# Kernel tuning notes

Measured on AMD Instinct MI355X. Metric: run time of the kernel, lower is better.

The kernel has to match this reference:

```python
import jax, jax.numpy as jnp
import numpy as np

B, S, H, D_IN, DEPTH, NPHN = 128, 1024, 256, 84, 2, 40
N_HEADS = 9  # phn, word1-3, utt1-5
EPS = 1e-5


def setup_inputs() -> dict:
    key = jax.random.key(0)
    ks = jax.random.split(key, 12)
    sc = 0.02
    x = jax.random.normal(ks[0], (B, S, D_IN), jnp.float32)
    # contiguous valid prefix then -1 padding (matches get_last_valid's assumption)
    lengths = jax.random.randint(ks[1], (B,), 1, S + 1)
    phn_vals = jax.random.randint(ks[2], (B, S), 0, NPHN - 1)
    phn = jnp.where(jnp.arange(S)[None, :] < lengths[:, None], phn_vals, -1)
    return {
        "x": x,
        "phn": phn,
        "in_proj_w": jax.random.normal(ks[3], (H, D_IN), jnp.float32) * sc,
        "in_proj_b": jnp.zeros((H,), jnp.float32),
        "phn_proj_w": jax.random.normal(ks[4], (H, NPHN), jnp.float32) * sc,
        "phn_proj_b": jnp.zeros((H,), jnp.float32),
        "w_ih": jax.random.normal(ks[5], (DEPTH, 4 * H, H), jnp.float32) * sc,
        "w_hh": jax.random.normal(ks[6], (DEPTH, 4 * H, H), jnp.float32) * sc,
        "b_ih": jnp.zeros((DEPTH, 4 * H), jnp.float32),
        "b_hh": jnp.zeros((DEPTH, 4 * H), jnp.float32),
        "ln_g": jnp.ones((N_HEADS, H), jnp.float32),
        "ln_b": jnp.zeros((N_HEADS, H), jnp.float32),
        "head_w": jax.random.normal(ks[7], (N_HEADS, H), jnp.float32) * sc,
        "head_b": jnp.zeros((N_HEADS,), jnp.float32),
    }


def _lstm(h0, w_ih, w_hh, b_ih, b_hh):
    # h0: [B,S,H]; torch gate order i,f,g,o
    seq = jnp.transpose(h0, (1, 0, 2))  # [S,B,H]
    b = h0.shape[0]
    for layer in range(DEPTH):
        Wih, Whh = w_ih[layer], w_hh[layer]
        bias = b_ih[layer] + b_hh[layer]

        def step(carry, xt, Wih=Wih, Whh=Whh, bias=bias):
            hp, cp = carry
            g = xt @ Wih.T + hp @ Whh.T + bias
            i, f, gg, o = jnp.split(g, 4, axis=-1)
            c = jax.nn.sigmoid(f) * cp + jax.nn.sigmoid(i) * jnp.tanh(gg)
            hn = jax.nn.sigmoid(o) * jnp.tanh(c)
            return (hn, c), hn

        init = (jnp.zeros((b, H), h0.dtype), jnp.zeros((b, H), h0.dtype))
        _, seq = jax.lax.scan(step, init, seq)
    return jnp.transpose(seq, (1, 0, 2))  # [B,S,H]


def reference(x, phn, in_proj_w, in_proj_b, phn_proj_w, phn_proj_b,
              w_ih, w_hh, b_ih, b_hh, ln_g, ln_b, head_w, head_b):
    b, s = x.shape[0], x.shape[1]
    mask = phn >= 0  # [B,S]
    phn_oh = jax.nn.one_hot(phn + 1, NPHN, dtype=x.dtype)
    h = (x @ in_proj_w.T + in_proj_b) + (phn_oh @ phn_proj_w.T + phn_proj_b)
    hidden = _lstm(h, w_ih, w_hh, b_ih, b_hh)  # [B,S,H]

    # All 9 heads share the LN-normalized activations; fold gamma/beta into the
    # per-head linear: score_k = <xhat, gamma_k*w_k> + <beta_k, w_k> + b_k
    mu = hidden.mean(-1, keepdims=True)
    var = ((hidden - mu) ** 2).mean(-1, keepdims=True)
    xhat = (hidden - mu) * jax.lax.rsqrt(var + EPS)
    scores = (jnp.einsum('bsh,kh->bsk', xhat, ln_g * head_w)
              + (ln_b * head_w).sum(-1) + head_b)  # [B,S,9]

    # last valid token per sequence: index before first mask==0 (or S-1 if all valid)
    first_inv = jnp.argmax(~mask, axis=1)
    idx = jnp.where(mask.all(axis=1), s - 1, first_inv - 1)  # [B]
    last = scores[jnp.arange(b), idx]  # [B,9]

    p = scores[..., 0:1]
    w1, w2, w3 = scores[..., 1:2], scores[..., 2:3], scores[..., 3:4]
    u1, u2, u3, u4, u5 = (last[:, 4 + k][:, None] for k in range(5))
    return (u1, u2, u3, u4, u5, p, w1, w2, w3)
```

## Files before the change

kernel.cpp:

```cpp
#include <hip/hip_runtime.h>


typedef _Float16 h2    __attribute__((ext_vector_type(2)));
typedef _Float16 f16x8 __attribute__((ext_vector_type(8)));
typedef float    f32x4 __attribute__((ext_vector_type(4)));

#define NW_MAT 262144

static __device__ __forceinline__ float fdot2u(unsigned int w, unsigned int h, float c){
#if defined(__has_builtin) && __has_builtin(__builtin_amdgcn_fdot2)
  return __builtin_amdgcn_fdot2(__builtin_bit_cast(h2, w), __builtin_bit_cast(h2, h), c, false);
#else
  h2 a = __builtin_bit_cast(h2, w), b = __builtin_bit_cast(h2, h);
  return c + (float)a[0]*(float)b[0] + (float)a[1]*(float)b[1];
#endif
}
static __device__ __forceinline__ float sigmf(float x){ return 1.f/(1.f + __expf(-x)); }
static __device__ __forceinline__ float tanhf_(float x){ return 1.f - 2.f/(__expf(2.f*x) + 1.f); }

__global__ void k_prep(const float* __restrict__ w_ih, const float* __restrict__ w_hh,
                       const float* __restrict__ b_ih, const float* __restrict__ b_hh,
                       const float* __restrict__ ln_g, const float* __restrict__ ln_b,
                       const float* __restrict__ head_w, const float* __restrict__ head_b,
                       _Float16* wih0, _Float16* whh0, _Float16* wih1, _Float16* whh1,
                       float* bias0, float* bias1, float* vk, float* ck)
{
  int i = blockIdx.x*256 + threadIdx.x;
  if (i < NW_MAT){
    wih0[i] = (_Float16)w_ih[i];
    whh0[i] = (_Float16)w_hh[i];
    wih1[i] = (_Float16)w_ih[NW_MAT + i];
    whh1[i] = (_Float16)w_hh[NW_MAT + i];
  }
  if (i < 1024){
    bias0[i] = b_ih[i]        + b_hh[i];
    bias1[i] = b_ih[1024 + i] + b_hh[1024 + i];
  }
  if (i < 2304) vk[i] = ln_g[i]*head_w[i];
  if (i < 9){
    float s = 0.f;
    for (int h = 0; h < 256; ++h) s += ln_b[i*256 + h]*head_w[i*256 + h];
    ck[i] = s + head_b[i];
  }
}

__global__ void k_idx(const int* __restrict__ phn, int* __restrict__ idx)
{
  int b = blockIdx.x, l = threadIdx.x;
  int found = -1;
  for (int t0 = 0; t0 < 1024; t0 += 64){
    int v = phn[b*1024 + t0 + l];
    unsigned long long m = __ballot(v < 0);
    if (m){ found = t0 + (__ffsll(m) - 1); break; }
  }
  if (l == 0) idx[b] = (found < 0) ? 1023 : found - 1;
}

__global__ void k_embed(const float* __restrict__ x, const int* __restrict__ phn,
                        const float* __restrict__ ipw, const float* __restrict__ ipb,
                        const float* __restrict__ ppw, const float* __restrict__ ppb,
                        _Float16* __restrict__ E, int Tc, int LT, int tc0)
{
  __shared__ float xs[8][84];
  __shared__ int pv[8];
  int tid = threadIdx.x;
  int m0 = blockIdx.x * 8;
  for (int i = tid; i < 8*84; i += 256){
    int r = i/84, k = i - r*84;
    int m = m0 + r; int b = m >> LT; int t = tc0 + (m & (Tc-1));
    xs[r][k] = x[((size_t)b*1024 + t)*84 + k];
  }
  if (tid < 8){
    int m = m0 + tid; int b = m >> LT; int t = tc0 + (m & (Tc-1));
    pv[tid] = phn[b*1024 + t];
  }
  __syncthreads();
  float acc[8] = {0.f,0.f,0.f,0.f,0.f,0.f,0.f,0.f};
  const float* wrow = ipw + tid*84;
  for (int k = 0; k < 84; ++k){
    float wv = wrow[k];
    #pragma unroll
    for (int r = 0; r < 8; ++r) acc[r] += wv * xs[r][k];
  }
  float base = ipb[tid] + ppb[tid];
  #pragma unroll
  for (int r = 0; r < 8; ++r){
    float e = acc[r] + base + ppw[tid*40 + (pv[r] + 1)];
    E[(size_t)(m0 + r)*256 + tid] = (_Float16)e;
  }
}

__global__ __launch_bounds__(256) void k_gemm(const _Float16* __restrict__ A,
                                              const _Float16* __restrict__ Bw,
                                              const float* __restrict__ bias,
                                              _Float16* __restrict__ C)
{
  __shared__ __align__(16) _Float16 lA[128*64];
  __shared__ __align__(16) _Float16 lB[128*64];
  int tid = threadIdx.x;
  int tm = blockIdx.x, tn = blockIdx.y;
  int l = tid & 63, w = tid >> 6;
  int wm = w >> 1, wn = w & 1;
  f32x4 acc[4][4];
  #pragma unroll
  for (int mi = 0; mi < 4; ++mi)
    #pragma unroll
    for (int ni = 0; ni < 4; ++ni) acc[mi][ni] = (f32x4){0.f,0.f,0.f,0.f};
  int rr = tid >> 3, cc = tid & 7;
  #pragma unroll 1
  for (int kb = 0; kb < 4; ++kb){
    uint4 av[4], bv[4];
    #pragma unroll
    for (int i = 0; i < 4; ++i){
      int r = rr + 32*i;
      av[i] = *(const uint4*)(A  + ((size_t)(tm*128 + r))*256 + kb*64 + cc*8);
      bv[i] = *(const uint4*)(Bw + ((size_t)(tn*128 + r))*256 + kb*64 + cc*8);
    }
    __syncthreads();
    #pragma unroll
    for (int i = 0; i < 4; ++i){
      int r = rr + 32*i;
      *(uint4*)&lA[r*64 + cc*8] = av[i];
      *(uint4*)&lB[r*64 + cc*8] = bv[i];
    }
    __syncthreads();
    #pragma unroll
    for (int kk = 0; kk < 2; ++kk){
      f16x8 aF[4], bF[4];
      #pragma unroll
      for (int mi = 0; mi < 4; ++mi)
        aF[mi] = *(const f16x8*)&lA[(wm*64 + mi*16 + (l&15))*64 + kk*32 + (l>>4)*8];
      #pragma unroll
      for (int ni = 0; ni < 4; ++ni)
        bF[ni] = *(const f16x8*)&lB[(wn*64 + ni*16 + (l&15))*64 + kk*32 + (l>>4)*8];
      #pragma unroll
      for (int mi = 0; mi < 4; ++mi)
        #pragma unroll
        for (int ni = 0; ni < 4; ++ni)
          acc[mi][ni] = __builtin_amdgcn_mfma_f32_16x16x32_f16(aF[mi], bF[ni], acc[mi][ni], 0, 0, 0);
    }
  }
  #pragma unroll
  for (int mi = 0; mi < 4; ++mi){
    #pragma unroll
    for (int ni = 0; ni < 4; ++ni){
      int n = tn*128 + wn*64 + ni*16 + (l & 15);
      float bn = bias[n];
      #pragma unroll
      for (int j = 0; j < 4; ++j){
        int m = tm*128 + wm*64 + mi*16 + (l>>4)*4 + j;
        C[(size_t)m*1024 + n] = (_Float16)(acc[mi][ni][j] + bn);
      }
    }
  }
}

__global__ __launch_bounds__(512, 2) void k_lstm(const _Float16* __restrict__ G,
                                                 const _Float16* __restrict__ W,
                                                 _Float16* __restrict__ Hout,
                                                 float* __restrict__ h_state,
                                                 float* __restrict__ c_state,
                                                 int Tc, int first)
{
  __shared__ __align__(16) unsigned int h_pk_s[128];
  __shared__ float gf[1024];
  __shared__ __align__(16) unsigned int wlds[32768];
  int tid = threadIdx.x;
  int b = blockIdx.x;
  int r0 = 2*tid, r1 = r0 + 1;
  const uint4* w0s = (const uint4*)(W + (size_t)r0*256);
  const uint4* w1s = (const uint4*)(W + (size_t)r1*256);
  uint4 w0v[24], w1v[24];
  #pragma unroll
  for (int c2 = 0; c2 < 24; ++c2){ w0v[c2] = w0s[c2]; w1v[c2] = w1s[c2]; }
  unsigned int swz = (unsigned int)(tid & 7);
  #pragma unroll
  for (int c2 = 0; c2 < 8; ++c2){
    *(uint4*)&wlds[tid*64      + (((unsigned)c2 ^ swz)*4)] = w0s[24 + c2];
    *(uint4*)&wlds[tid*64 + 32 + (((unsigned)c2 ^ swz)*4)] = w1s[24 + c2];
  }
  float c_reg = 0.f, hn = 0.f;
  if (tid < 256){
    float hv = 0.f;
    if (!first){ hv = h_state[b*256 + tid]; c_reg = c_state[b*256 + tid]; }
    ((_Float16*)h_pk_s)[tid] = (_Float16)hv;
    hn = hv;
  }
  __syncthreads();
  const unsigned int* gbase = (const unsigned int*)G + (size_t)b*Tc*512 + tid;
  _Float16* hout = Hout + (size_t)b*Tc*256;
  unsigned int gc = gbase[0];
  for (int tl = 0; tl < Tc; ++tl){
    unsigned int gn = (tl + 1 < Tc) ? gbase[(size_t)(tl + 1)*512] : 0u;
    const uint4* hp = (const uint4*)h_pk_s;
    float acc0 = 0.f, acc1 = 0.f;
    #pragma unroll
    for (int c2 = 0; c2 < 24; ++c2){
      uint4 h4 = hp[c2];
      acc0 = fdot2u(w0v[c2].x, h4.x, acc0);
      acc0 = fdot2u(w0v[c2].y, h4.y, acc0);
      acc0 = fdot2u(w0v[c2].z, h4.z, acc0);
      acc0 = fdot2u(w0v[c2].w, h4.w, acc0);
      acc1 = fdot2u(w1v[c2].x, h4.x, acc1);
      acc1 = fdot2u(w1v[c2].y, h4.y, acc1);
      acc1 = fdot2u(w1v[c2].z, h4.z, acc1);
      acc1 = fdot2u(w1v[c2].w, h4.w, acc1);
    }
    #pragma unroll
    for (int c2 = 0; c2 < 8; ++c2){
      uint4 wv0 = *(const uint4*)&wlds[tid*64      + (((unsigned)c2 ^ swz)*4)];
      uint4 wv1 = *(const uint4*)&wlds[tid*64 + 32 + (((unsigned)c2 ^ swz)*4)];
      uint4 h4 = hp[24 + c2];
      acc0 = fdot2u(wv0.x, h4.x, acc0);
      acc0 = fdot2u(wv0.y, h4.y, acc0);
      acc0 = fdot2u(wv0.z, h4.z, acc0);
      acc0 = fdot2u(wv0.w, h4.w, acc0);
      acc1 = fdot2u(wv1.x, h4.x, acc1);
      acc1 = fdot2u(wv1.y, h4.y, acc1);
      acc1 = fdot2u(wv1.z, h4.z, acc1);
      acc1 = fdot2u(wv1.w, h4.w, acc1);
    }
    h2 gp = __builtin_bit_cast(h2, gc);
    gf[r0] = acc0 + (float)gp[0];
    gf[r1] = acc1 + (float)gp[1];
    __syncthreads();
    if (tid < 256){
      float gi = gf[tid], gfr = gf[tid + 256], gg = gf[tid + 512], go = gf[tid + 768];
      float ct = sigmf(gfr)*c_reg + sigmf(gi)*tanhf_(gg);
      c_reg = ct;
      hn = sigmf(go)*tanhf_(ct);
      ((_Float16*)h_pk_s)[tid] = (_Float16)hn;
      hout[(size_t)tl*256 + tid] = (_Float16)hn;
    }
    __syncthreads();
    gc = gn;
  }
  if (tid < 256){ h_state[b*256 + tid] = hn; c_state[b*256 + tid] = c_reg; }
}

__global__ void k_ln(const _Float16* __restrict__ H1, const float* __restrict__ vk,
                     const float* __restrict__ ck, const int* __restrict__ idx,
                     float* __restrict__ out, int Tc, int LT, int tc0)
{
  __shared__ __align__(16) float vks[9*256];
  __shared__ float cks[9];
  int tid = threadIdx.x;
  for (int i = tid; i < 2304; i += 256) vks[i] = vk[i];
  if (tid < 9) cks[tid] = ck[tid];
  __syncthreads();
  int l = tid & 63, wv = tid >> 6;
  int m = blockIdx.x*4 + wv;
  int b = m >> LT; int t = tc0 + (m & (Tc-1));
  uint2 hv = *(const uint2*)(H1 + (size_t)m*256 + l*4);
  h2 pa = __builtin_bit_cast(h2, hv.x), pb = __builtin_bit_cast(h2, hv.y);
  float f0 = pa[0], f1 = pa[1], f2 = pb[0], f3 = pb[1];
  float s = f0 + f1 + f2 + f3;
  float q = f0*f0 + f1*f1 + f2*f2 + f3*f3;
  #pragma unroll
  for (int o = 32; o > 0; o >>= 1){ s += __shfl_xor(s, o, 64); q += __shfl_xor(q, o, 64); }
  float mu = s*(1.f/256.f);
  float var = q*(1.f/256.f) - mu*mu;
  float rstd = rsqrtf(var + 1e-5f);
  float xh0 = (f0 - mu)*rstd, xh1 = (f1 - mu)*rstd, xh2 = (f2 - mu)*rstd, xh3 = (f3 - mu)*rstd;
  int ib = idx[b];
  size_t rout = (size_t)b*1024 + t;
  #pragma unroll 1
  for (int k = 0; k < 9; ++k){
    float4 vvv = *(const float4*)(vks + k*256 + l*4);
    float p = xh0*vvv.x + xh1*vvv.y + xh2*vvv.z + xh3*vvv.w;
    #pragma unroll
    for (int o = 32; o > 0; o >>= 1) p += __shfl_xor(p, o, 64);
    if (l == 0){
      float sc = p + cks[k];
      if (k < 4) out[640 + (size_t)k*131072 + rout] = sc;
      else if (t == ib) out[(k - 4)*128 + b] = sc;
    }
  }
}

extern "C" void kernel_launch(void* const* d_in, const int* in_sizes, int n_in,
                              void* d_out, int out_size, void* d_ws, size_t ws_size,
                              hipStream_t stream)
{
  const float* x      = (const float*)d_in[0];
  const int*   phn    = (const int*)  d_in[1];
  const float* in_w   = (const float*)d_in[2];
  const float* in_b   = (const float*)d_in[3];
  const float* ph_w   = (const float*)d_in[4];
  const float* ph_b   = (const float*)d_in[5];
  const float* w_ih   = (const float*)d_in[6];
  const float* w_hh   = (const float*)d_in[7];
  const float* b_ih   = (const float*)d_in[8];
  const float* b_hh   = (const float*)d_in[9];
  const float* ln_g   = (const float*)d_in[10];
  const float* ln_b   = (const float*)d_in[11];
  const float* head_w = (const float*)d_in[12];
  const float* head_b = (const float*)d_in[13];
  float* out = (float*)d_out;
  char* wsb = (char*)d_ws;
  size_t o = 0;
  auto take = [&](size_t n) -> char* { char* p = wsb + o; o = (o + n + 255) & ~(size_t)255; return p; };
  _Float16* wih0 = (_Float16*)take(524288);
  _Float16* whh0 = (_Float16*)take(524288);
  _Float16* wih1 = (_Float16*)take(524288);
  _Float16* whh1 = (_Float16*)take(524288);
  float* bias0 = (float*)take(4096);
  float* bias1 = (float*)take(4096);
  float* vk    = (float*)take(9216);
  float* ck    = (float*)take(64);
  int*   idxb  = (int*)take(512);
  float* h0s = (float*)take(131072);
  float* c0s = (float*)take(131072);
  float* h1s = (float*)take(131072);
  float* c1s = (float*)take(131072);
  const size_t per_t = 3*(size_t)65536 + 1048576;
  int Tc = 1024;
  while (Tc > 8 && o + (size_t)Tc*per_t > ws_size) Tc >>= 1;
  _Float16* Eb  = (_Float16*)take((size_t)Tc*65536);
  _Float16* H0b = (_Float16*)take((size_t)Tc*65536);
  _Float16* H1b = (_Float16*)take((size_t)Tc*65536);
  _Float16* Gb  = (_Float16*)take((size_t)Tc*1048576);
  int LT = __builtin_ctz((unsigned)Tc);

  k_prep<<<1024, 256, 0, stream>>>(w_ih, w_hh, b_ih, b_hh, ln_g, ln_b, head_w, head_b,
                                   wih0, whh0, wih1, whh1, bias0, bias1, vk, ck);
  k_idx<<<128, 64, 0, stream>>>(phn, idxb);

  int M = 128*Tc;
  int nchunks = 1024/Tc;
  for (int c = 0; c < nchunks; ++c){
    int tc0 = c*Tc;
    k_embed<<<M/8, 256, 0, stream>>>(x, phn, in_w, in_b, ph_w, ph_b, Eb, Tc, LT, tc0);
    k_gemm<<<dim3(M/128, 8), 256, 0, stream>>>(Eb, wih0, bias0, Gb);
    k_lstm<<<128, 512, 0, stream>>>(Gb, whh0, H0b, h0s, c0s, Tc, c == 0 ? 1 : 0);
    k_gemm<<<dim3(M/128, 8), 256, 0, stream>>>(H0b, wih1, bias1, Gb);
    k_lstm<<<128, 512, 0, stream>>>(Gb, whh1, H1b, h1s, c1s, Tc, c == 0 ? 1 : 0);
    k_ln<<<M/4, 256, 0, stream>>>(H1b, vk, ck, idxb, out, Tc, LT, tc0);
  }
  (void)in_sizes; (void)n_in; (void)out_size;
}
```

Before: 5.560 ms.

## Split LSTM recurrence across 4 blocks per batch pair with global barrier sync

The recurrent LSTM kernel now uses 256 blocks instead of 128. Each group of 4 blocks shares two batch rows and each block owns a 64-unit slice of all four gates. Because the slice is smaller, the whole recurrent weight slice fits in LDS rather than being held in registers. At every timestep the new hidden state is exchanged through double-buffered global memory and an atomic counter barrier between the four blocks. This aims to shorten the per-step dot-product critical path and use more CUs, at the cost of a cross-block spin barrier each step, which needs all 256 blocks co-resident.

```diff
diff --git a/kernel.cpp b/kernel.cpp
--- a/kernel.cpp
+++ b/kernel.cpp
@@ -155,87 +155,97 @@
   }
 }
 
-__global__ __launch_bounds__(512, 2) void k_lstm(const _Float16* __restrict__ G,
-                                                 const _Float16* __restrict__ W,
-                                                 _Float16* __restrict__ Hout,
-                                                 float* __restrict__ h_state,
-                                                 float* __restrict__ c_state,
-                                                 int Tc, int first)
-{
-  __shared__ __align__(16) unsigned int h_pk_s[128];
-  __shared__ float gf[1024];
-  __shared__ __align__(16) unsigned int wlds[32768];
+__global__ __launch_bounds__(512)
+void k_lstm_g(const _Float16* __restrict__ G,
+              const _Float16* __restrict__ W,
+              _Float16* __restrict__ Hout,
+              float* __restrict__ h_state,
+              float* __restrict__ c_state,
+              float* __restrict__ hx0, float* __restrict__ hx1,
+              unsigned int* __restrict__ cnt,
+              int Tc, int first, int epoch_base)
+{
+  __shared__ __align__(16) unsigned int Wl[33792];
+  __shared__ __align__(16) unsigned int hl[256];
+  __shared__ float gl[512];
   int tid = threadIdx.x;
-  int b = blockIdx.x;
-  int r0 = 2*tid, r1 = r0 + 1;
-  const uint4* w0s = (const uint4*)(W + (size_t)r0*256);
-  const uint4* w1s = (const uint4*)(W + (size_t)r1*256);
-  uint4 w0v[24], w1v[24];
-  #pragma unroll
-  for (int c2 = 0; c2 < 24; ++c2){ w0v[c2] = w0s[c2]; w1v[c2] = w1s[c2]; }
-  unsigned int swz = (unsigned int)(tid & 7);
-  #pragma unroll
-  for (int c2 = 0; c2 < 8; ++c2){
-    *(uint4*)&wlds[tid*64      + (((unsigned)c2 ^ swz)*4)] = w0s[24 + c2];
-    *(uint4*)&wlds[tid*64 + 32 + (((unsigned)c2 ^ swz)*4)] = w1s[24 + c2];
-  }
+  int bid = blockIdx.x;
+  int s = bid >> 6, g = bid & 63;
+  int lr = tid >> 1, cw = tid & 1;
+  int gate = lr >> 6, ul = lr & 63;
+  int u = s*64 + ul;
+  int grow = gate*256 + u;
+  {
+    const uint4* wg = (const uint4*)(W + (size_t)grow*256);
+    uint4* wl4 = (uint4*)Wl;
+    #pragma unroll
+    for (int kk = 0; kk < 16; ++kk)
+      wl4[lr*33 + cw*16 + kk] = wg[cw*16 + kk];
+  }
+  {
+    int ccg = tid >> 8, uu = tid & 255;
+    float hv = first ? 0.f : h_state[(g*2 + ccg)*256 + uu];
+    ((_Float16*)hl)[ccg*256 + uu] = (_Float16)hv;
+  }
+  int co = (tid >> 6) & 1, uo = tid & 63;
   float c_reg = 0.f, hn = 0.f;
-  if (tid < 256){
-    float hv = 0.f;
-    if (!first){ hv = h_state[b*256 + tid]; c_reg = c_state[b*256 + tid]; }
-    ((_Float16*)h_pk_s)[tid] = (_Float16)hv;
-    hn = hv;
+  if (tid < 128 && !first){
+    c_reg = c_state[(g*2 + co)*256 + s*64 + uo];
+    hn    = h_state[(g*2 + co)*256 + s*64 + uo];
   }
   __syncthreads();
-  const unsigned int* gbase = (const unsigned int*)G + (size_t)b*Tc*512 + tid;
-  _Float16* hout = Hout + (size_t)b*Tc*256;
-  unsigned int gc = gbase[0];
+  const _Float16* gsrc = G + ((size_t)(g*2 + cw)*Tc)*1024 + grow;
+  _Float16* hout_o = Hout + ((size_t)(g*2 + co)*Tc)*256 + s*64 + uo;
+  #pragma unroll 1
   for (int tl = 0; tl < Tc; ++tl){
-    unsigned int gn = (tl + 1 < Tc) ? gbase[(size_t)(tl + 1)*512] : 0u;
-    const uint4* hp = (const uint4*)h_pk_s;
-    float acc0 = 0.f, acc1 = 0.f;
-    #pragma unroll
-    for (int c2 = 0; c2 < 24; ++c2){
-      uint4 h4 = hp[c2];
-      acc0 = fdot2u(w0v[c2].x, h4.x, acc0);
-      acc0 = fdot2u(w0v[c2].y, h4.y, acc0);
-      acc0 = fdot2u(w0v[c2].z, h4.z, acc0);
-      acc0 = fdot2u(w0v[c2].w, h4.w, acc0);
-      acc1 = fdot2u(w1v[c2].x, h4.x, acc1);
-      acc1 = fdot2u(w1v[c2].y, h4.y, acc1);
-      acc1 = fdot2u(w1v[c2].z, h4.z, acc1);
-      acc1 = fdot2u(w1v[c2].w, h4.w, acc1);
-    }
-    #pragma unroll
-    for (int c2 = 0; c2 < 8; ++c2){
-      uint4 wv0 = *(const uint4*)&wlds[tid*64      + (((unsigned)c2 ^ swz)*4)];
-      uint4 wv1 = *(const uint4*)&wlds[tid*64 + 32 + (((unsigned)c2 ^ swz)*4)];
-      uint4 h4 = hp[24 + c2];
-      acc0 = fdot2u(wv0.x, h4.x, acc0);
-      acc0 = fdot2u(wv0.y, h4.y, acc0);
-      acc0 = fdot2u(wv0.z, h4.z, acc0);
-      acc0 = fdot2u(wv0.w, h4.w, acc0);
-      acc1 = fdot2u(wv1.x, h4.x, acc1);
-      acc1 = fdot2u(wv1.y, h4.y, acc1);
-      acc1 = fdot2u(wv1.z, h4.z, acc1);
-      acc1 = fdot2u(wv1.w, h4.w, acc1);
-    }
-    h2 gp = __builtin_bit_cast(h2, gc);
-    gf[r0] = acc0 + (float)gp[0];
-    gf[r1] = acc1 + (float)gp[1];
-    __syncthreads();
-    if (tid < 256){
-      float gi = gf[tid], gfr = gf[tid + 256], gg = gf[tid + 512], go = gf[tid + 768];
+    float gx = (float)gsrc[(size_t)tl*1024];
+    const uint4* wrow = (const uint4*)Wl + lr*33;
+    const uint4* hrow = (const uint4*)hl + cw*32;
+    float a0 = 0.f, a1 = 0.f;
+    #pragma unroll
+    for (int j = 0; j < 32; j += 2){
+      uint4 w4 = wrow[j],   h4 = hrow[j];
+      uint4 w5 = wrow[j+1], h5 = hrow[j+1];
+      a0 = fdot2u(w4.x, h4.x, a0); a0 = fdot2u(w4.y, h4.y, a0);
+      a0 = fdot2u(w4.z, h4.z, a0); a0 = fdot2u(w4.w, h4.w, a0);
+      a1 = fdot2u(w5.x, h5.x, a1); a1 = fdot2u(w5.y, h5.y, a1);
+      a1 = fdot2u(w5.z, h5.z, a1); a1 = fdot2u(w5.w, h5.w, a1);
+    }
+    gl[cw*256 + lr] = a0 + a1 + gx;
+    __syncthreads();
+    int epoch = epoch_base + tl;
+    float* hx = (epoch & 1) ? hx1 : hx0;
+    if (tid < 128){
+      float gi  = gl[co*256 + uo],       gfr = gl[co*256 + 64 + uo];
+      float gg  = gl[co*256 + 128 + uo], go  = gl[co*256 + 192 + uo];
       float ct = sigmf(gfr)*c_reg + sigmf(gi)*tanhf_(gg);
       c_reg = ct;
       hn = sigmf(go)*tanhf_(ct);
-      ((_Float16*)h_pk_s)[tid] = (_Float16)hn;
-      hout[(size_t)tl*256 + tid] = (_Float16)hn;
-    }
-    __syncthreads();
-    gc = gn;
-  }
-  if (tid < 256){ h_state[b*256 + tid] = hn; c_state[b*256 + tid] = c_reg; }
+      hout_o[(size_t)tl*256] = (_Float16)hn;
+      __hip_atomic_store(&hx[(g*2 + co)*256 + s*64 + uo], hn,
+                         __ATOMIC_RELAXED, __HIP_MEMORY_SCOPE_AGENT);
+    }
+    __syncthreads();
+    if (tid == 0){
+      __hip_atomic_fetch_add(&cnt[g*32], 1u, __ATOMIC_RELEASE, __HIP_MEMORY_SCOPE_AGENT);
+      unsigned int tgt = 4u*(unsigned)(epoch + 1);
+      while (__hip_atomic_load(&cnt[g*32], __ATOMIC_RELAXED, __HIP_MEMORY_SCOPE_AGENT) < tgt)
+        __builtin_amdgcn_s_sleep(1);
+      (void)__hip_atomic_load(&cnt[g*32], __ATOMIC_ACQUIRE, __HIP_MEMORY_SCOPE_AGENT);
+    }
+    __syncthreads();
+    {
+      int ccg = tid >> 8, uu = tid & 255;
+      float hv = __hip_atomic_load(&hx[(g*2 + ccg)*256 + uu],
+                                   __ATOMIC_RELAXED, __HIP_MEMORY_SCOPE_AGENT);
+      ((_Float16*)hl)[ccg*256 + uu] = (_Float16)hv;
+    }
+    __syncthreads();
+  }
+  if (tid < 128){
+    h_state[(g*2 + co)*256 + s*64 + uo] = hn;
+    c_state[(g*2 + co)*256 + s*64 + uo] = c_reg;
+  }
 }
 
 __global__ void k_ln(const _Float16* __restrict__ H1, const float* __restrict__ vk,
@@ -313,6 +323,9 @@
   float* c0s = (float*)take(131072);
   float* h1s = (float*)take(131072);
   float* c1s = (float*)take(131072);
+  float* hx0 = (float*)take(131072);
+  float* hx1 = (float*)take(131072);
+  unsigned int* cntp = (unsigned int*)take(8192);
   const size_t per_t = 3*(size_t)65536 + 1048576;
   int Tc = 1024;
   while (Tc > 8 && o + (size_t)Tc*per_t > ws_size) Tc >>= 1;
@@ -322,19 +335,25 @@
   _Float16* Gb  = (_Float16*)take((size_t)Tc*1048576);
   int LT = __builtin_ctz((unsigned)Tc);
 
+  hipMemsetAsync(cntp, 0, 8192, stream);
   k_prep<<<1024, 256, 0, stream>>>(w_ih, w_hh, b_ih, b_hh, ln_g, ln_b, head_w, head_b,
                                    wih0, whh0, wih1, whh1, bias0, bias1, vk, ck);
   k_idx<<<128, 64, 0, stream>>>(phn, idxb);
 
   int M = 128*Tc;
   int nchunks = 1024/Tc;
+  int epoch_base = 0;
   for (int c = 0; c < nchunks; ++c){
     int tc0 = c*Tc;
     k_embed<<<M/8, 256, 0, stream>>>(x, phn, in_w, in_b, ph_w, ph_b, Eb, Tc, LT, tc0);
     k_gemm<<<dim3(M/128, 8), 256, 0, stream>>>(Eb, wih0, bias0, Gb);
-    k_lstm<<<128, 512, 0, stream>>>(Gb, whh0, H0b, h0s, c0s, Tc, c == 0 ? 1 : 0);
+    k_lstm_g<<<256, 512, 0, stream>>>(Gb, whh0, H0b, h0s, c0s, hx0, hx1, cntp,
+                                      Tc, c == 0 ? 1 : 0, epoch_base);
+    epoch_base += Tc;
     k_gemm<<<dim3(M/128, 8), 256, 0, stream>>>(H0b, wih1, bias1, Gb);
-    k_lstm<<<128, 512, 0, stream>>>(Gb, whh1, H1b, h1s, c1s, Tc, c == 0 ? 1 : 0);
+    k_lstm_g<<<256, 512, 0, stream>>>(Gb, whh1, H1b, h1s, c1s, hx0, hx1, cntp,
+                                      Tc, c == 0 ? 1 : 0, epoch_base);
+    epoch_base += Tc;
     k_ln<<<M/4, 256, 0, stream>>>(H1b, vk, ck, idxb, out, Tc, LT, tc0);
   }
   (void)in_sizes; (void)n_in; (void)out_size;
```

New measurement: 11.78 ms. +111.9%, slower.
